# Kernel tuning notes

Hardware: AMD Instinct MI355X
Metric: run time of the kernel (lower is better)

The kernel has to match this reference:

```python
import jax, jax.numpy as jnp
import numpy as np

N = 4096          # N_TARGET_NODES (node count == feature dim)
E = 262144        # number of directed edges (avg degree 64)


def setup_inputs() -> dict:
    key = jax.random.key(0)
    k1, k2, k3, k4 = jax.random.split(key, 4)
    x = jax.random.normal(k1, (N, N), dtype=jnp.float32)
    edge_index = jax.random.randint(k2, (2, E), 0, N, dtype=jnp.int32)
    # scale weights so sigmoid inputs are O(1)
    W1 = jax.random.normal(k3, (N, N), dtype=jnp.float32) * (1.0 / np.sqrt(N))
    b1 = jnp.zeros((N,), dtype=jnp.float32)
    W2 = jax.random.normal(k4, (N, 1), dtype=jnp.float32) * (1.0 / np.sqrt(N))
    b2 = jnp.zeros((1,), dtype=jnp.float32)
    return {"x": x, "edge_index": edge_index, "W1": W1, "b1": b1, "W2": W2, "b2": b2}


def _gcn_conv(x, edge_index, W, b):
    """PyG GCNConv: h = D^{-1/2}(A+I)D^{-1/2} (x W) + b, edge weights = 1."""
    n = x.shape[0]
    h = x @ W                                   # [n, out]
    loop = jnp.arange(n, dtype=edge_index.dtype)
    src = jnp.concatenate([edge_index[0], loop])  # add self loops
    dst = jnp.concatenate([edge_index[1], loop])
    deg = jax.ops.segment_sum(jnp.ones_like(src, dtype=h.dtype), dst, num_segments=n)
    dinv = jnp.where(deg > 0, jax.lax.rsqrt(deg), 0.0)
    norm = dinv[src] * dinv[dst]                # [E+n]
    msg = h[src] * norm[:, None]                # gather + scale
    out = jax.ops.segment_sum(msg, dst, num_segments=n)  # scatter-add at targets
    return out + b


def reference(x, edge_index, W1, b1, W2, b2):
    # torch.squeeze(x) is a no-op for 2-D x
    x1 = jax.nn.sigmoid(_gcn_conv(x, edge_index, W1, b1))
    # F.dropout in eval mode is identity (deterministic reference)
    x2 = jax.nn.sigmoid(_gcn_conv(x1, edge_index, W2, b2))
    return x2  # [N, 1]
```

## Files before the change

### kernel.cpp

```cpp
#include <hip/hip_runtime.h>


typedef __attribute__((ext_vector_type(8))) short bf16x8;
typedef __attribute__((ext_vector_type(4))) float f32x4;

#define NN 4096
#define NT 64

__device__ __forceinline__ unsigned f2bf(float f) {
  unsigned u = __float_as_uint(f);
  return (u + 0x7FFFu + ((u >> 16) & 1u)) >> 16;
}

#define GLDS(g, l) __builtin_amdgcn_global_load_lds(                      \
    (const __attribute__((address_space(1))) void*)(g),                   \
    (__attribute__((address_space(3))) void*)(l), 16, 0, 0)


__global__ void init_deg_kernel(float* deg) {
  int v = blockIdx.x * 256 + threadIdx.x;
  if (v < NN) deg[v] = 1.0f;
}

__global__ void count_deg_kernel(const int* __restrict__ dst, int E, float* deg) {
  int e = blockIdx.x * 256 + threadIdx.x;
  if (e < E) atomicAdd(&deg[dst[e]], 1.0f);
}

__global__ void dinv_kernel(const float* __restrict__ deg, float* __restrict__ dinv) {
  int v = blockIdx.x * 256 + threadIdx.x;
  if (v < NN) dinv[v] = rsqrtf(deg[v]);
}

__global__ void diag_bf16_kernel(const float* __restrict__ dinv, unsigned short* __restrict__ Sbf) {
  int v = blockIdx.x * 256 + threadIdx.x;
  if (v < NN) { float d = dinv[v]; Sbf[(size_t)v * NN + v] = (unsigned short)f2bf(d * d); }
}

__global__ void scatter_bf16_kernel(const int* __restrict__ src, const int* __restrict__ dst,
                                    int E, const float* __restrict__ dinv,
                                    unsigned int* __restrict__ Sw) {
  int e = blockIdx.x * 256 + threadIdx.x;
  if (e >= E) return;
  int s = src[e], d = dst[e];
  float val = dinv[s] * dinv[d];
  size_t idx = (size_t)d * NN + s;
  unsigned int* p = Sw + (idx >> 1);
  const bool hi = (idx & 1) != 0;
  unsigned old = *p, assumed;
  do {
    assumed = old;
    unsigned short cur = hi ? (unsigned short)(assumed >> 16) : (unsigned short)(assumed & 0xFFFFu);
    float f = __uint_as_float(((unsigned)cur) << 16) + val;
    unsigned short nb = (unsigned short)f2bf(f);
    unsigned nw = hi ? ((assumed & 0x0000FFFFu) | ((unsigned)nb << 16))
                     : ((assumed & 0xFFFF0000u) | (unsigned)nb);
    old = atomicCAS(p, assumed, nw);
  } while (old != assumed);
}


__global__ void cast_kernel(const float* __restrict__ in, unsigned short* __restrict__ out, int n) {
  int i = (blockIdx.x * 256 + threadIdx.x) * 8;
  if (i >= n) return;
  const float4* p = (const float4*)(in + i);
  float4 a = p[0], b = p[1];
  uint4 o;
  o.x = f2bf(a.x) | (f2bf(a.y) << 16);
  o.y = f2bf(a.z) | (f2bf(a.w) << 16);
  o.z = f2bf(b.x) | (f2bf(b.y) << 16);
  o.w = f2bf(b.z) | (f2bf(b.w) << 16);
  *(uint4*)(out + i) = o;
}

__global__ void transpose_cast_kernel(const float* __restrict__ W, unsigned short* __restrict__ WT) {
  __shared__ float tile[64][65];
  const int tid = threadIdx.x;
  const int bx = blockIdx.x * 64, by = blockIdx.y * 64;
  const int tx = tid & 63, ty = tid >> 6;
#pragma unroll
  for (int i = 0; i < 64; i += 4)
    tile[ty + i][tx] = W[(size_t)(by + ty + i) * NN + bx + tx];
  __syncthreads();
  const int wtx = tid & 15, wty = tid >> 4;
#pragma unroll
  for (int i = 0; i < 64; i += 16) {
    int r = wty + i;
    ushort4 v;
    v.x = (unsigned short)f2bf(tile[4 * wtx + 0][r]);
    v.y = (unsigned short)f2bf(tile[4 * wtx + 1][r]);
    v.z = (unsigned short)f2bf(tile[4 * wtx + 2][r]);
    v.w = (unsigned short)f2bf(tile[4 * wtx + 3][r]);
    *(ushort4*)(WT + (size_t)(bx + r) * NN + by + 4 * wtx) = v;
  }
}


template <int EPI>
__global__ __launch_bounds__(512, 2) void gemm256_kernel(
    const unsigned short* __restrict__ A, const unsigned short* __restrict__ BT,
    unsigned short* __restrict__ C, const float* __restrict__ bias,
    const float* __restrict__ W2, float* __restrict__ h2) {
  __shared__ __align__(16) char smem[131072];
  const int tid = threadIdx.x;
  const int lane = tid & 63, wid = tid >> 6;
  const int wr = wid >> 2, wc = wid & 3;

  const int bid = blockIdx.x;
  const int swz = (bid & 7) * 32 + (bid >> 3);
  const int rowBase = (swz >> 4) * 256;
  const int colBase = (swz & 15) * 256;

  const int srow = tid >> 3;
  const int scolb = ((tid & 7) << 4) ^ ((srow & 7) << 4);
  const unsigned short* pA = A + (size_t)(rowBase + srow) * NN + (scolb >> 1);
  const unsigned short* pB = BT + (size_t)(colBase + srow) * NN + (scolb >> 1);

  const int rl = lane & 15;
  const int c0 = ((lane >> 4) << 4) ^ ((lane & 7) << 4);
  const int c1 = c0 ^ 64;
  const int aoff = (wr * 128 + rl) * 128;
  const int boff = 32768 + (wc * 64 + rl) * 128;

  f32x4 acc[8][4] = {};
  bf16x8 bk0[4], bk1[4], afA[4], afB[4];

  {
    char* w0 = smem + (wid << 10);
    GLDS(pB + (size_t)0 * 64 * NN, w0 + 32768 + 0 * 8192);
    GLDS(pB + (size_t)1 * 64 * NN, w0 + 32768 + 1 * 8192);
    GLDS(pB + (size_t)2 * 64 * NN, w0 + 32768 + 2 * 8192);
    GLDS(pB + (size_t)3 * 64 * NN, w0 + 32768 + 3 * 8192);
    GLDS(pA + (size_t)0 * 64 * NN, w0 + 0 * 8192);
    GLDS(pA + (size_t)2 * 64 * NN, w0 + 2 * 8192);
    GLDS(pA + (size_t)1 * 64 * NN, w0 + 1 * 8192);
    GLDS(pA + (size_t)3 * 64 * NN, w0 + 3 * 8192);
    asm volatile("s_waitcnt vmcnt(2)" ::: "memory");
    __builtin_amdgcn_s_barrier();
#pragma unroll
    for (int m = 0; m < 4; ++m) afA[m] = *(const bf16x8*)(smem + aoff + m * 2048 + c0);
#pragma unroll
    for (int n = 0; n < 4; ++n) bk0[n] = *(const bf16x8*)(smem + boff + n * 2048 + c0);
  }

#pragma unroll 2
  for (int t = 0; t < NT; ++t) {
    const char* lb = smem + ((t & 1) << 16);
    char* st = smem + (((t & 1) ^ 1) << 16) + (wid << 10);
    const unsigned short* s1A = pA + (size_t)(t + 1) * 64;
    const unsigned short* s1B = pB + (size_t)(t + 1) * 64;

    GLDS(s1B + (size_t)0 * 64 * NN, st + 32768 + 0 * 8192);
    GLDS(s1B + (size_t)1 * 64 * NN, st + 32768 + 1 * 8192);
    GLDS(s1B + (size_t)2 * 64 * NN, st + 32768 + 2 * 8192);
#pragma unroll
    for (int m = 0; m < 4; ++m) afB[m] = *(const bf16x8*)(lb + aoff + m * 2048 + c1);
#pragma unroll
    for (int n = 0; n < 4; ++n) bk1[n] = *(const bf16x8*)(lb + boff + n * 2048 + c1);
    __builtin_amdgcn_s_setprio(1);
#pragma unroll
    for (int m = 0; m < 4; ++m)
#pragma unroll
      for (int n = 0; n < 4; ++n)
        acc[m][n] = __builtin_amdgcn_mfma_f32_16x16x32_bf16(afA[m], bk0[n], acc[m][n], 0, 0, 0);
    __builtin_amdgcn_s_setprio(0);
    asm volatile("s_waitcnt vmcnt(3)" ::: "memory");
    __builtin_amdgcn_sched_barrier(0);

    GLDS(s1B + (size_t)3 * 64 * NN, st + 32768 + 3 * 8192);
    GLDS(s1A + (size_t)0 * 64 * NN, st + 0 * 8192);
    GLDS(s1A + (size_t)2 * 64 * NN, st + 2 * 8192);
#pragma unroll
    for (int m = 0; m < 4; ++m) afA[m] = *(const bf16x8*)(lb + aoff + (4 + m) * 2048 + c0);
    __builtin_amdgcn_s_setprio(1);
#pragma unroll
    for (int m = 0; m < 4; ++m)
#pragma unroll
      for (int n = 0; n < 4; ++n)
        acc[m][n] = __builtin_amdgcn_mfma_f32_16x16x32_bf16(afB[m], bk1[n], acc[m][n], 0, 0, 0);
    __builtin_amdgcn_s_setprio(0);
    __builtin_amdgcn_sched_barrier(0);

    GLDS(s1A + (size_t)1 * 64 * NN, st + 1 * 8192);
    GLDS(s1A + (size_t)3 * 64 * NN, st + 3 * 8192);
#pragma unroll
    for (int m = 0; m < 4; ++m) afB[m] = *(const bf16x8*)(lb + aoff + (4 + m) * 2048 + c1);
    __builtin_amdgcn_s_setprio(1);
#pragma unroll
    for (int m = 0; m < 4; ++m)
#pragma unroll
      for (int n = 0; n < 4; ++n)
        acc[4 + m][n] = __builtin_amdgcn_mfma_f32_16x16x32_bf16(afA[m], bk0[n], acc[4 + m][n], 0, 0, 0);
    __builtin_amdgcn_s_setprio(0);
    asm volatile("s_waitcnt lgkmcnt(0)" ::: "memory");
    asm volatile("s_waitcnt vmcnt(2)" ::: "memory");
    __builtin_amdgcn_s_barrier();
    __builtin_amdgcn_sched_barrier(0);

    {
      const char* nb = smem + (((t + 1) & 1) << 16);
#pragma unroll
      for (int m = 0; m < 4; ++m) afA[m] = *(const bf16x8*)(nb + aoff + m * 2048 + c0);
#pragma unroll
      for (int n = 0; n < 4; ++n) bk0[n] = *(const bf16x8*)(nb + boff + n * 2048 + c0);
    }
    __builtin_amdgcn_s_setprio(1);
#pragma unroll
    for (int m = 0; m < 4; ++m)
#pragma unroll
      for (int n = 0; n < 4; ++n)
        acc[4 + m][n] = __builtin_amdgcn_mfma_f32_16x16x32_bf16(afB[m], bk1[n], acc[4 + m][n], 0, 0, 0);
    __builtin_amdgcn_s_setprio(0);
    __builtin_amdgcn_sched_barrier(0);
  }

  const int orow = rowBase + wr * 128 + (lane >> 4) * 4;
  const int ocol = colBase + wc * 64 + (lane & 15);
  if (EPI == 0) {
#pragma unroll
    for (int n = 0; n < 4; ++n) {
      int ccol = ocol + n * 16;
#pragma unroll
      for (int m = 0; m < 8; ++m) {
#pragma unroll
        for (int i = 0; i < 4; ++i) {
          C[(size_t)(orow + m * 16 + i) * NN + ccol] = (unsigned short)f2bf(acc[m][n][i]);
        }
      }
    }
  } else {
    float bv[4], wv[4];
#pragma unroll
    for (int n = 0; n < 4; ++n) { bv[n] = bias[ocol + n * 16]; wv[n] = W2[ocol + n * 16]; }
#pragma unroll
    for (int m = 0; m < 8; ++m) {
#pragma unroll
      for (int i = 0; i < 4; ++i) {
        float s = 0.0f;
#pragma unroll
        for (int n = 0; n < 4; ++n) {
          float x = 1.0f / (1.0f + __expf(-(acc[m][n][i] + bv[n])));
          s += x * wv[n];
        }
        s += __shfl_xor(s, 1);
        s += __shfl_xor(s, 2);
        s += __shfl_xor(s, 4);
        s += __shfl_xor(s, 8);
        if ((lane & 15) == 0) atomicAdd(&h2[orow + m * 16 + i], s);
      }
    }
  }
}


__global__ void init_t_kernel(const float* __restrict__ dinv, const float* __restrict__ h2,
                              const float* __restrict__ b2, float* __restrict__ tacc) {
  int v = blockIdx.x * 256 + threadIdx.x;
  if (v < NN) tacc[v] = dinv[v] * dinv[v] * h2[v] + b2[0];
}

__global__ void scatter_t_kernel(const int* __restrict__ src, const int* __restrict__ dst,
                                 int E, const float* __restrict__ dinv,
                                 const float* __restrict__ h2, float* __restrict__ tacc) {
  int e = blockIdx.x * 256 + threadIdx.x;
  if (e < E) {
    int s = src[e], d = dst[e];
    atomicAdd(&tacc[d], dinv[s] * dinv[d] * h2[s]);
  }
}

__global__ void final_kernel(const float* __restrict__ tacc, float* __restrict__ out) {
  int v = blockIdx.x * 256 + threadIdx.x;
  if (v < NN) out[v] = 1.0f / (1.0f + __expf(-tacc[v]));
}


extern "C" void kernel_launch(void* const* d_in, const int* in_sizes, int n_in,
                              void* d_out, int out_size, void* d_ws, size_t ws_size,
                              hipStream_t stream) {
  const float* x  = (const float*)d_in[0];
  const int*   ei = (const int*)d_in[1];
  const float* W1 = (const float*)d_in[2];
  const float* b1 = (const float*)d_in[3];
  const float* W2 = (const float*)d_in[4];
  const float* b2 = (const float*)d_in[5];
  float* out = (float*)d_out;
  const int E = in_sizes[1] / 2;
  const int* esrc = ei;
  const int* edst = ei + E;

  char* w = (char*)d_ws;
  unsigned short* H1T = (unsigned short*)w;
  unsigned short* W1T = (unsigned short*)(w + (size_t)(32u << 20));
  unsigned short* Sbf = (unsigned short*)(w + (size_t)(64u << 20));
  unsigned short* Xbf = (unsigned short*)(w + (size_t)(96u << 20));
  float* deg  = (float*)(w + (size_t)(128u << 20));
  float* dinv = deg + 4096;
  float* h2   = deg + 8192;
  float* tacc = deg + 12288;

  init_deg_kernel<<<16, 256, 0, stream>>>(deg);
  count_deg_kernel<<<(E + 255) / 256, 256, 0, stream>>>(edst, E, deg);
  dinv_kernel<<<16, 256, 0, stream>>>(deg, dinv);

  hipMemsetAsync(Sbf, 0, (size_t)32 << 20, stream);
  hipMemsetAsync(h2, 0, 4096 * sizeof(float), stream);
  diag_bf16_kernel<<<16, 256, 0, stream>>>(dinv, Sbf);
  scatter_bf16_kernel<<<(E + 255) / 256, 256, 0, stream>>>(esrc, edst, E, dinv,
                                                           (unsigned int*)Sbf);

  cast_kernel<<<8192, 256, 0, stream>>>(x, Xbf, NN * NN);
  transpose_cast_kernel<<<dim3(64, 64), 256, 0, stream>>>(W1, W1T);

  gemm256_kernel<0><<<256, 512, 0, stream>>>(W1T, Xbf, H1T, nullptr, nullptr, nullptr);
  gemm256_kernel<1><<<256, 512, 0, stream>>>(Sbf, H1T, nullptr, b1, W2, h2);

  init_t_kernel<<<16, 256, 0, stream>>>(dinv, h2, b2, tacc);
  scatter_t_kernel<<<(E + 255) / 256, 256, 0, stream>>>(esrc, edst, E, dinv, h2, tacc);
  final_kernel<<<16, 256, 0, stream>>>(tacc, out);
}
```

Measured before the change: 324.8 us.

## Switch GEMM to 32x32x16 MFMA and fuse preprocessing into one kernel

The GEMM's inner product moves from 16x16x32 to 32x32x16 bf16 MFMA tiles, with new LDS fragment offsets and a rewritten epilogue. This aims to raise matrix-core throughput and cut LDS reads per FLOP. Separately, the edge scatter, x cast, W1 transpose-cast and diagonal write are merged into one launch. The dinv, init_deg and init_t kernels are removed by computing rsqrt(deg+1) inline and folding the self-loop term into the final kernel. This cuts launch count and small-kernel overhead but complicates the code and changes the accumulator layout.

```diff
diff --git a/kernel.cpp b/kernel.cpp
--- a/kernel.cpp
+++ b/kernel.cpp
@@ -2,7 +2,7 @@
 
 
 typedef __attribute__((ext_vector_type(8))) short bf16x8;
-typedef __attribute__((ext_vector_type(4))) float f32x4;
+typedef __attribute__((ext_vector_type(16))) float f32x16;
 
 #define NN 4096
 #define NT 64
@@ -17,81 +17,69 @@
     (__attribute__((address_space(3))) void*)(l), 16, 0, 0)
 
 
-__global__ void init_deg_kernel(float* deg) {
-  int v = blockIdx.x * 256 + threadIdx.x;
-  if (v < NN) deg[v] = 1.0f;
-}
-
 __global__ void count_deg_kernel(const int* __restrict__ dst, int E, float* deg) {
   int e = blockIdx.x * 256 + threadIdx.x;
   if (e < E) atomicAdd(&deg[dst[e]], 1.0f);
 }
 
-__global__ void dinv_kernel(const float* __restrict__ deg, float* __restrict__ dinv) {
-  int v = blockIdx.x * 256 + threadIdx.x;
-  if (v < NN) dinv[v] = rsqrtf(deg[v]);
-}
-
-__global__ void diag_bf16_kernel(const float* __restrict__ dinv, unsigned short* __restrict__ Sbf) {
-  int v = blockIdx.x * 256 + threadIdx.x;
-  if (v < NN) { float d = dinv[v]; Sbf[(size_t)v * NN + v] = (unsigned short)f2bf(d * d); }
-}
-
-__global__ void scatter_bf16_kernel(const int* __restrict__ src, const int* __restrict__ dst,
-                                    int E, const float* __restrict__ dinv,
-                                    unsigned int* __restrict__ Sw) {
-  int e = blockIdx.x * 256 + threadIdx.x;
-  if (e >= E) return;
-  int s = src[e], d = dst[e];
-  float val = dinv[s] * dinv[d];
-  size_t idx = (size_t)d * NN + s;
-  unsigned int* p = Sw + (idx >> 1);
-  const bool hi = (idx & 1) != 0;
-  unsigned old = *p, assumed;
-  do {
-    assumed = old;
-    unsigned short cur = hi ? (unsigned short)(assumed >> 16) : (unsigned short)(assumed & 0xFFFFu);
-    float f = __uint_as_float(((unsigned)cur) << 16) + val;
-    unsigned short nb = (unsigned short)f2bf(f);
-    unsigned nw = hi ? ((assumed & 0x0000FFFFu) | ((unsigned)nb << 16))
-                     : ((assumed & 0xFFFF0000u) | (unsigned)nb);
-    old = atomicCAS(p, assumed, nw);
-  } while (old != assumed);
-}
-
-
-__global__ void cast_kernel(const float* __restrict__ in, unsigned short* __restrict__ out, int n) {
-  int i = (blockIdx.x * 256 + threadIdx.x) * 8;
-  if (i >= n) return;
-  const float4* p = (const float4*)(in + i);
-  float4 a = p[0], b = p[1];
-  uint4 o;
-  o.x = f2bf(a.x) | (f2bf(a.y) << 16);
-  o.y = f2bf(a.z) | (f2bf(a.w) << 16);
-  o.z = f2bf(b.x) | (f2bf(b.y) << 16);
-  o.w = f2bf(b.z) | (f2bf(b.w) << 16);
-  *(uint4*)(out + i) = o;
-}
-
-__global__ void transpose_cast_kernel(const float* __restrict__ W, unsigned short* __restrict__ WT) {
-  __shared__ float tile[64][65];
-  const int tid = threadIdx.x;
-  const int bx = blockIdx.x * 64, by = blockIdx.y * 64;
-  const int tx = tid & 63, ty = tid >> 6;
-#pragma unroll
-  for (int i = 0; i < 64; i += 4)
-    tile[ty + i][tx] = W[(size_t)(by + ty + i) * NN + bx + tx];
-  __syncthreads();
-  const int wtx = tid & 15, wty = tid >> 4;
-#pragma unroll
-  for (int i = 0; i < 64; i += 16) {
-    int r = wty + i;
-    ushort4 v;
-    v.x = (unsigned short)f2bf(tile[4 * wtx + 0][r]);
-    v.y = (unsigned short)f2bf(tile[4 * wtx + 1][r]);
-    v.z = (unsigned short)f2bf(tile[4 * wtx + 2][r]);
-    v.w = (unsigned short)f2bf(tile[4 * wtx + 3][r]);
-    *(ushort4*)(WT + (size_t)(bx + r) * NN + by + 4 * wtx) = v;
+
+__global__ void prep_kernel(const int* __restrict__ src, const int* __restrict__ dst, int E,
+                            const float* __restrict__ deg,
+                            unsigned int* __restrict__ Sw, unsigned short* __restrict__ Sbf,
+                            const float* __restrict__ x, unsigned short* __restrict__ Xbf,
+                            const float* __restrict__ W1, unsigned short* __restrict__ W1T) {
+  const int bid = blockIdx.x, tid = threadIdx.x;
+  if (bid < 1024) {
+    int e = bid * 256 + tid;
+    if (e >= E) return;
+    int s = src[e], d = dst[e];
+    float val = rsqrtf(deg[s] + 1.0f) * rsqrtf(deg[d] + 1.0f);
+    size_t idx = (size_t)d * NN + s;
+    unsigned int* p = Sw + (idx >> 1);
+    const bool hi = (idx & 1) != 0;
+    unsigned old = *p, assumed;
+    do {
+      assumed = old;
+      unsigned short cur = hi ? (unsigned short)(assumed >> 16) : (unsigned short)(assumed & 0xFFFFu);
+      float f = __uint_as_float(((unsigned)cur) << 16) + val;
+      unsigned short nb = (unsigned short)f2bf(f);
+      unsigned nw = hi ? ((assumed & 0x0000FFFFu) | ((unsigned)nb << 16))
+                       : ((assumed & 0xFFFF0000u) | (unsigned)nb);
+      old = atomicCAS(p, assumed, nw);
+    } while (old != assumed);
+  } else if (bid < 9216) {
+    int i = ((bid - 1024) * 256 + tid) * 8;
+    const float4* p = (const float4*)(x + i);
+    float4 a = p[0], b = p[1];
+    uint4 o;
+    o.x = f2bf(a.x) | (f2bf(a.y) << 16);
+    o.y = f2bf(a.z) | (f2bf(a.w) << 16);
+    o.z = f2bf(b.x) | (f2bf(b.y) << 16);
+    o.w = f2bf(b.z) | (f2bf(b.w) << 16);
+    *(uint4*)(Xbf + i) = o;
+  } else if (bid < 13312) {
+    __shared__ float tile[64][65];
+    const int t = bid - 9216;
+    const int bx = (t & 63) * 64, by = (t >> 6) * 64;
+    const int tx = tid & 63, ty = tid >> 6;
+#pragma unroll
+    for (int i = 0; i < 64; i += 4)
+      tile[ty + i][tx] = W1[(size_t)(by + ty + i) * NN + bx + tx];
+    __syncthreads();
+    const int wtx = tid & 15, wty = tid >> 4;
+#pragma unroll
+    for (int i = 0; i < 64; i += 16) {
+      int r = wty + i;
+      ushort4 v;
+      v.x = (unsigned short)f2bf(tile[4 * wtx + 0][r]);
+      v.y = (unsigned short)f2bf(tile[4 * wtx + 1][r]);
+      v.z = (unsigned short)f2bf(tile[4 * wtx + 2][r]);
+      v.w = (unsigned short)f2bf(tile[4 * wtx + 3][r]);
+      *(ushort4*)(W1T + (size_t)(bx + r) * NN + by + 4 * wtx) = v;
+    }
+  } else {
+    int v = (bid - 13312) * 256 + tid;
+    if (v < NN) Sbf[(size_t)v * NN + v] = (unsigned short)f2bf(1.0f / (deg[v] + 1.0f));
   }
 }
 
@@ -116,13 +104,13 @@
   const unsigned short* pA = A + (size_t)(rowBase + srow) * NN + (scolb >> 1);
   const unsigned short* pB = BT + (size_t)(colBase + srow) * NN + (scolb >> 1);
 
-  const int rl = lane & 15;
-  const int c0 = ((lane >> 4) << 4) ^ ((lane & 7) << 4);
-  const int c1 = c0 ^ 64;
-  const int aoff = (wr * 128 + rl) * 128;
-  const int boff = 32768 + (wc * 64 + rl) * 128;
-
-  f32x4 acc[8][4] = {};
+  const int l31 = lane & 31, l5 = lane >> 5;
+  const int c0 = ((l5 ^ (lane & 7)) << 4);
+  const int c1 = c0 ^ 32, c2 = c0 ^ 64, c3 = c0 ^ 96;
+  const int aoff = (wr * 128 + l31) * 128;
+  const int boff = 32768 + (wc * 64 + l31) * 128;
+
+  f32x16 acc[4][2] = {};
   bf16x8 bk0[4], bk1[4], afA[4], afB[4];
 
   {
@@ -137,11 +125,28 @@
     GLDS(pA + (size_t)3 * 64 * NN, w0 + 3 * 8192);
     asm volatile("s_waitcnt vmcnt(2)" ::: "memory");
     __builtin_amdgcn_s_barrier();
-#pragma unroll
-    for (int m = 0; m < 4; ++m) afA[m] = *(const bf16x8*)(smem + aoff + m * 2048 + c0);
-#pragma unroll
-    for (int n = 0; n < 4; ++n) bk0[n] = *(const bf16x8*)(smem + boff + n * 2048 + c0);
-  }
+    afA[0] = *(const bf16x8*)(smem + aoff + 0 * 4096 + c0);
+    afA[1] = *(const bf16x8*)(smem + aoff + 0 * 4096 + c1);
+    afA[2] = *(const bf16x8*)(smem + aoff + 1 * 4096 + c0);
+    afA[3] = *(const bf16x8*)(smem + aoff + 1 * 4096 + c1);
+    bk0[0] = *(const bf16x8*)(smem + boff + 0 * 4096 + c0);
+    bk0[1] = *(const bf16x8*)(smem + boff + 0 * 4096 + c1);
+    bk0[2] = *(const bf16x8*)(smem + boff + 1 * 4096 + c0);
+    bk0[3] = *(const bf16x8*)(smem + boff + 1 * 4096 + c1);
+  }
+
+#define MFMA8(AF, BK, MH)                                                              \
+  _Pragma("unroll")                                                                    \
+  for (int mb = 0; mb < 2; ++mb)                                                       \
+    _Pragma("unroll")                                                                  \
+    for (int nb = 0; nb < 2; ++nb) {                                                   \
+      acc[MH * 2 + mb][nb] =                                                           \
+          __builtin_amdgcn_mfma_f32_32x32x16_bf16(AF[mb * 2 + 0], BK[nb * 2 + 0],      \
+                                                  acc[MH * 2 + mb][nb], 0, 0, 0);      \
+      acc[MH * 2 + mb][nb] =                                                           \
+          __builtin_amdgcn_mfma_f32_32x32x16_bf16(AF[mb * 2 + 1], BK[nb * 2 + 1],      \
+                                                  acc[MH * 2 + mb][nb], 0, 0, 0);      \
+    }
 
 #pragma unroll 2
   for (int t = 0; t < NT; ++t) {
@@ -153,16 +158,16 @@
     GLDS(s1B + (size_t)0 * 64 * NN, st + 32768 + 0 * 8192);
     GLDS(s1B + (size_t)1 * 64 * NN, st + 32768 + 1 * 8192);
     GLDS(s1B + (size_t)2 * 64 * NN, st + 32768 + 2 * 8192);
-#pragma unroll
-    for (int m = 0; m < 4; ++m) afB[m] = *(const bf16x8*)(lb + aoff + m * 2048 + c1);
-#pragma unroll
-    for (int n = 0; n < 4; ++n) bk1[n] = *(const bf16x8*)(lb + boff + n * 2048 + c1);
+    afB[0] = *(const bf16x8*)(lb + aoff + 0 * 4096 + c2);
+    afB[1] = *(const bf16x8*)(lb + aoff + 0 * 4096 + c3);
+    afB[2] = *(const bf16x8*)(lb + aoff + 1 * 4096 + c2);
+    afB[3] = *(const bf16x8*)(lb + aoff + 1 * 4096 + c3);
+    bk1[0] = *(const bf16x8*)(lb + boff + 0 * 4096 + c2);
+    bk1[1] = *(const bf16x8*)(lb + boff + 0 * 4096 + c3);
+    bk1[2] = *(const bf16x8*)(lb + boff + 1 * 4096 + c2);
+    bk1[3] = *(const bf16x8*)(lb + boff + 1 * 4096 + c3);
     __builtin_amdgcn_s_setprio(1);
-#pragma unroll
-    for (int m = 0; m < 4; ++m)
-#pragma unroll
-      for (int n = 0; n < 4; ++n)
-        acc[m][n] = __builtin_amdgcn_mfma_f32_16x16x32_bf16(afA[m], bk0[n], acc[m][n], 0, 0, 0);
+    MFMA8(afA, bk0, 0)
     __builtin_amdgcn_s_setprio(0);
     asm volatile("s_waitcnt vmcnt(3)" ::: "memory");
     __builtin_amdgcn_sched_barrier(0);
@@ -170,27 +175,23 @@
     GLDS(s1B + (size_t)3 * 64 * NN, st + 32768 + 3 * 8192);
     GLDS(s1A + (size_t)0 * 64 * NN, st + 0 * 8192);
     GLDS(s1A + (size_t)2 * 64 * NN, st + 2 * 8192);
-#pragma unroll
-    for (int m = 0; m < 4; ++m) afA[m] = *(const bf16x8*)(lb + aoff + (4 + m) * 2048 + c0);
+    afA[0] = *(const bf16x8*)(lb + aoff + 2 * 4096 + c0);
+    afA[1] = *(const bf16x8*)(lb + aoff + 2 * 4096 + c1);
+    afA[2] = *(const bf16x8*)(lb + aoff + 3 * 4096 + c0);
+    afA[3] = *(const bf16x8*)(lb + aoff + 3 * 4096 + c1);
     __builtin_amdgcn_s_setprio(1);
-#pragma unroll
-    for (int m = 0; m < 4; ++m)
-#pragma unroll
-      for (int n = 0; n < 4; ++n)
-        acc[m][n] = __builtin_amdgcn_mfma_f32_16x16x32_bf16(afB[m], bk1[n], acc[m][n], 0, 0, 0);
+    MFMA8(afB, bk1, 0)
     __builtin_amdgcn_s_setprio(0);
     __builtin_amdgcn_sched_barrier(0);
 
     GLDS(s1A + (size_t)1 * 64 * NN, st + 1 * 8192);
     GLDS(s1A + (size_t)3 * 64 * NN, st + 3 * 8192);
-#pragma unroll
-    for (int m = 0; m < 4; ++m) afB[m] = *(const bf16x8*)(lb + aoff + (4 + m) * 2048 + c1);
+    afB[0] = *(const bf16x8*)(lb + aoff + 2 * 4096 + c2);
+    afB[1] = *(const bf16x8*)(lb + aoff + 2 * 4096 + c3);
+    afB[2] = *(const bf16x8*)(lb + aoff + 3 * 4096 + c2);
+    afB[3] = *(const bf16x8*)(lb + aoff + 3 * 4096 + c3);
     __builtin_amdgcn_s_setprio(1);
-#pragma unroll
-    for (int m = 0; m < 4; ++m)
-#pragma unroll
-      for (int n = 0; n < 4; ++n)
-        acc[4 + m][n] = __builtin_amdgcn_mfma_f32_16x16x32_bf16(afA[m], bk0[n], acc[4 + m][n], 0, 0, 0);
+    MFMA8(afA, bk0, 1)
     __builtin_amdgcn_s_setprio(0);
     asm volatile("s_waitcnt lgkmcnt(0)" ::: "memory");
     asm volatile("s_waitcnt vmcnt(2)" ::: "memory");
@@ -198,80 +199,73 @@
     __builtin_amdgcn_sched_barrier(0);
 
     {
-      const char* nb = smem + (((t + 1) & 1) << 16);
-#pragma unroll
-      for (int m = 0; m < 4; ++m) afA[m] = *(const bf16x8*)(nb + aoff + m * 2048 + c0);
-#pragma unroll
-      for (int n = 0; n < 4; ++n) bk0[n] = *(const bf16x8*)(nb + boff + n * 2048 + c0);
+      const char* nb_ = smem + (((t + 1) & 1) << 16);
+      afA[0] = *(const bf16x8*)(nb_ + aoff + 0 * 4096 + c0);
+      afA[1] = *(const bf16x8*)(nb_ + aoff + 0 * 4096 + c1);
+      afA[2] = *(const bf16x8*)(nb_ + aoff + 1 * 4096 + c0);
+      afA[3] = *(const bf16x8*)(nb_ + aoff + 1 * 4096 + c1);
+      bk0[0] = *(const bf16x8*)(nb_ + boff + 0 * 4096 + c0);
+      bk0[1] = *(const bf16x8*)(nb_ + boff + 0 * 4096 + c1);
+      bk0[2] = *(const bf16x8*)(nb_ + boff + 1 * 4096 + c0);
+      bk0[3] = *(const bf16x8*)(nb_ + boff + 1 * 4096 + c1);
     }
     __builtin_amdgcn_s_setprio(1);
-#pragma unroll
-    for (int m = 0; m < 4; ++m)
-#pragma unroll
-      for (int n = 0; n < 4; ++n)
-        acc[4 + m][n] = __builtin_amdgcn_mfma_f32_16x16x32_bf16(afB[m], bk1[n], acc[4 + m][n], 0, 0, 0);
+    MFMA8(afB, bk1, 1)
     __builtin_amdgcn_s_setprio(0);
     __builtin_amdgcn_sched_barrier(0);
   }
 
-  const int orow = rowBase + wr * 128 + (lane >> 4) * 4;
-  const int ocol = colBase + wc * 64 + (lane & 15);
+  const int orowb = rowBase + wr * 128 + l5 * 4;
+  const int ocol = colBase + wc * 64 + l31;
   if (EPI == 0) {
 #pragma unroll
-    for (int n = 0; n < 4; ++n) {
-      int ccol = ocol + n * 16;
-#pragma unroll
-      for (int m = 0; m < 8; ++m) {
-#pragma unroll
-        for (int i = 0; i < 4; ++i) {
-          C[(size_t)(orow + m * 16 + i) * NN + ccol] = (unsigned short)f2bf(acc[m][n][i]);
+    for (int mb = 0; mb < 4; ++mb)
+#pragma unroll
+      for (int nb = 0; nb < 2; ++nb)
+#pragma unroll
+        for (int r = 0; r < 16; ++r) {
+          int row = orowb + mb * 32 + (r & 3) + 8 * (r >> 2);
+          C[(size_t)row * NN + ocol + nb * 32] = (unsigned short)f2bf(acc[mb][nb][r]);
         }
-      }
-    }
   } else {
-    float bv[4], wv[4];
-#pragma unroll
-    for (int n = 0; n < 4; ++n) { bv[n] = bias[ocol + n * 16]; wv[n] = W2[ocol + n * 16]; }
-#pragma unroll
-    for (int m = 0; m < 8; ++m) {
-#pragma unroll
-      for (int i = 0; i < 4; ++i) {
-        float s = 0.0f;
-#pragma unroll
-        for (int n = 0; n < 4; ++n) {
-          float x = 1.0f / (1.0f + __expf(-(acc[m][n][i] + bv[n])));
-          s += x * wv[n];
-        }
+    float bv0 = bias[ocol], bv1 = bias[ocol + 32];
+    float wv0 = W2[ocol], wv1 = W2[ocol + 32];
+#pragma unroll
+    for (int mb = 0; mb < 4; ++mb)
+#pragma unroll
+      for (int r = 0; r < 16; ++r) {
+        float s = wv0 / (1.0f + __expf(-(acc[mb][0][r] + bv0)))
+                + wv1 / (1.0f + __expf(-(acc[mb][1][r] + bv1)));
         s += __shfl_xor(s, 1);
         s += __shfl_xor(s, 2);
         s += __shfl_xor(s, 4);
         s += __shfl_xor(s, 8);
-        if ((lane & 15) == 0) atomicAdd(&h2[orow + m * 16 + i], s);
+        s += __shfl_xor(s, 16);
+        if (l31 == 0)
+          atomicAdd(&h2[orowb + mb * 32 + (r & 3) + 8 * (r >> 2)], s);
       }
-    }
-  }
-}
-
-
-__global__ void init_t_kernel(const float* __restrict__ dinv, const float* __restrict__ h2,
-                              const float* __restrict__ b2, float* __restrict__ tacc) {
-  int v = blockIdx.x * 256 + threadIdx.x;
-  if (v < NN) tacc[v] = dinv[v] * dinv[v] * h2[v] + b2[0];
-}
+  }
+}
+
 
 __global__ void scatter_t_kernel(const int* __restrict__ src, const int* __restrict__ dst,
-                                 int E, const float* __restrict__ dinv,
+                                 int E, const float* __restrict__ deg,
                                  const float* __restrict__ h2, float* __restrict__ tacc) {
   int e = blockIdx.x * 256 + threadIdx.x;
   if (e < E) {
     int s = src[e], d = dst[e];
-    atomicAdd(&tacc[d], dinv[s] * dinv[d] * h2[s]);
-  }
-}
-
-__global__ void final_kernel(const float* __restrict__ tacc, float* __restrict__ out) {
+    atomicAdd(&tacc[d], rsqrtf(deg[s] + 1.0f) * rsqrtf(deg[d] + 1.0f) * h2[s]);
+  }
+}
+
+__global__ void final_kernel(const float* __restrict__ tacc, const float* __restrict__ deg,
+                             const float* __restrict__ h2, const float* __restrict__ b2,
+                             float* __restrict__ out) {
   int v = blockIdx.x * 256 + threadIdx.x;
-  if (v < NN) out[v] = 1.0f / (1.0f + __expf(-tacc[v]));
+  if (v < NN) {
+    float tv = tacc[v] + h2[v] / (deg[v] + 1.0f) + b2[0];
+    out[v] = 1.0f / (1.0f + __expf(-tv));
+  }
 }
 
 
@@ -295,27 +289,20 @@
   unsigned short* Sbf = (unsigned short*)(w + (size_t)(64u << 20));
   unsigned short* Xbf = (unsigned short*)(w + (size_t)(96u << 20));
   float* deg  = (float*)(w + (size_t)(128u << 20));
-  float* dinv = deg + 4096;
-  float* h2   = deg + 8192;
-  float* tacc = deg + 12288;
-
-  init_deg_kernel<<<16, 256, 0, stream>>>(deg);
+  float* h2   = deg + 4096;
+  float* tacc = deg + 8192;
+
+  hipMemsetAsync(deg, 0, 3 * 4096 * sizeof(float), stream);
+  hipMemsetAsync(Sbf, 0, (size_t)32 << 20, stream);
+
   count_deg_kernel<<<(E + 255) / 256, 256, 0, stream>>>(edst, E, deg);
-  dinv_kernel<<<16, 256, 0, stream>>>(deg, dinv);
-
-  hipMemsetAsync(Sbf, 0, (size_t)32 << 20, stream);
-  hipMemsetAsync(h2, 0, 4096 * sizeof(float), stream);
-  diag_bf16_kernel<<<16, 256, 0, stream>>>(dinv, Sbf);
-  scatter_bf16_kernel<<<(E + 255) / 256, 256, 0, stream>>>(esrc, edst, E, dinv,
-                                                           (unsigned int*)Sbf);
-
-  cast_kernel<<<8192, 256, 0, stream>>>(x, Xbf, NN * NN);
-  transpose_cast_kernel<<<dim3(64, 64), 256, 0, stream>>>(W1, W1T);
+
+  prep_kernel<<<13328, 256, 0, stream>>>(esrc, edst, E, deg, (unsigned int*)Sbf, Sbf,
+                                         x, Xbf, W1, W1T);
 
   gemm256_kernel<0><<<256, 512, 0, stream>>>(W1T, Xbf, H1T, nullptr, nullptr, nullptr);
   gemm256_kernel<1><<<256, 512, 0, stream>>>(Sbf, H1T, nullptr, b1, W2, h2);
 
-  init_t_kernel<<<16, 256, 0, stream>>>(dinv, h2, b2, tacc);
-  scatter_t_kernel<<<(E + 255) / 256, 256, 0, stream>>>(esrc, edst, E, dinv, h2, tacc);
-  final_kernel<<<16, 256, 0, stream>>>(tacc, out);
-}
+  scatter_t_kernel<<<(E + 255) / 256, 256, 0, stream>>>(esrc, edst, E, deg, h2, tacc);
+  final_kernel<<<16, 256, 0, stream>>>(tacc, deg, h2, b2, out);
+}
```

Result: slower. 359.7 us (+10.7%).
